# Performance work log

Hardware: AMD Instinct MI355X
Metric: run time of the kernel (lower is better)

Reference implementation:

```python
import jax, jax.numpy as jnp
import numpy as np

B, N, C, H = 8, 1568, 384, 6
D = C // H
SCALE = D ** -0.5
EPS = 1e-6


def setup_inputs() -> dict:
    key = jax.random.key(0)
    k1, k2, k3, k4 = jax.random.split(key, 4)
    x = jax.random.normal(k1, (B, N, C), dtype=jnp.float32)
    # binary token-keep policy (0/1), as produced by the pruning module
    vis_tube = jax.random.randint(k2, (B, N, 1), 0, 2).astype(jnp.float32)
    w_qkv = jax.random.normal(k3, (3 * C, C), dtype=jnp.float32) * (C ** -0.5)
    w_proj = jax.random.normal(k4, (C, C), dtype=jnp.float32) * (C ** -0.5)
    b_proj = jnp.zeros((C,), dtype=jnp.float32)
    return {"x": x, "vis_tube": vis_tube, "w_qkv": w_qkv, "w_proj": w_proj, "b_proj": b_proj}


def _attn_forward(x, vis_tube, w_qkv, w_proj, b_proj):
    qkv = (x @ w_qkv.T).reshape(B, N, 3, H, D)
    qkv = jnp.transpose(qkv, (2, 0, 3, 1, 4))  # [3,B,H,N,D]
    q, k, v = qkv[0], qkv[1], qkv[2]

    attn = jnp.einsum('bhnd,bhmd->bhnm', q, k) * SCALE  # [B,H,N,N]

    # softmax_with_policy: mask keys by policy, but always keep the diagonal
    policy = vis_tube.reshape(B, 1, 1, N)
    eye = jnp.eye(N, dtype=policy.dtype).reshape(1, 1, N, N)
    attn_policy = policy + (1.0 - policy) * eye  # [B,1,N,N]

    max_att = jnp.max(attn, axis=-1, keepdims=True)
    e = jnp.exp(attn - max_att) * attn_policy
    attn = (e + EPS / N) / (jnp.sum(e, axis=-1, keepdims=True) + EPS)

    out = jnp.einsum('bhnm,bhmd->bhnd', attn, v)  # [B,H,N,D]
    out = jnp.transpose(out, (0, 2, 1, 3)).reshape(B, N, C)
    return out @ w_proj.T + b_proj


def reference(x, vis_tube, w_qkv, w_proj, b_proj):
    return _attn_forward(x, vis_tube, w_qkv, w_proj, b_proj)
```

## Files before the change

### kernel.cpp

```cpp
#include <hip/hip_runtime.h>

#define B_ 8
#define N_ 1568
#define C_ 384
#define H_ 6
#define D_ 64
#define BH_ 48
#define SZ_ (B_*H_*N_*D_)
#define EPS_ 1e-6f
#define EPSN_ (EPS_/(float)N_)
#define CSC_ 0.18033688011112042f

typedef short s16x8 __attribute__((ext_vector_type(8)));
typedef float f32x4 __attribute__((ext_vector_type(4)));

static __device__ __forceinline__ ushort f2bf(float f){
  union { float f; unsigned u; } v; v.f = f;
  unsigned r = v.u + 0x7fffu + ((v.u >> 16) & 1u);
  return (ushort)(r >> 16);
}
static __device__ __forceinline__ float bf2f(ushort u){
  union { unsigned u; float f; } v; v.u = ((unsigned)u) << 16; return v.f;
}
static __device__ __forceinline__ s16x8 pack8(float4 a, float4 b){
  s16x8 r;
  r[0]=(short)f2bf(a.x); r[1]=(short)f2bf(a.y); r[2]=(short)f2bf(a.z); r[3]=(short)f2bf(a.w);
  r[4]=(short)f2bf(b.x); r[5]=(short)f2bf(b.y); r[6]=(short)f2bf(b.z); r[7]=(short)f2bf(b.w);
  return r;
}
#define MFMA16(a,b,c) __builtin_amdgcn_mfma_f32_16x16x32_bf16((a),(b),(c),0,0,0)

#if __has_builtin(__builtin_amdgcn_exp2f)
#define EXP2F(x) __builtin_amdgcn_exp2f(x)
#else
#define EXP2F(x) exp2f(x)
#endif

#if __has_builtin(__builtin_amdgcn_update_dpp)
#define ROT16(x,c) __int_as_float(__builtin_amdgcn_update_dpp(0, __float_as_int(x), (c), 0xf, 0xf, true))
static __device__ __forceinline__ float rmax16(float x){
  x = fmaxf(x, ROT16(x,0x121)); x = fmaxf(x, ROT16(x,0x122));
  x = fmaxf(x, ROT16(x,0x124)); x = fmaxf(x, ROT16(x,0x128)); return x;
}
static __device__ __forceinline__ float rsum16(float x){
  x += ROT16(x,0x121); x += ROT16(x,0x122); x += ROT16(x,0x124); x += ROT16(x,0x128); return x;
}
#else
static __device__ __forceinline__ float rmax16(float x){
  x = fmaxf(x, __shfl_xor(x,1)); x = fmaxf(x, __shfl_xor(x,2));
  x = fmaxf(x, __shfl_xor(x,4)); x = fmaxf(x, __shfl_xor(x,8)); return x;
}
static __device__ __forceinline__ float rsum16(float x){
  x += __shfl_xor(x,1); x += __shfl_xor(x,2); x += __shfl_xor(x,4); x += __shfl_xor(x,8); return x;
}
#endif

__global__ __launch_bounds__(256) void qkv_gemm(const float* __restrict__ X, const float* __restrict__ W,
                                                ushort* __restrict__ Qg, ushort* __restrict__ Kg,
                                                ushort* __restrict__ Vg){
  __shared__ __align__(16) ushort Al[128*40];
  __shared__ __align__(16) ushort Bl[64*40];
  const int tid = threadIdx.x, lane = tid&63, w = tid>>6;
  const int g = lane>>4, lr = lane&15;
  const int wr = w>>1, wc = w&1;
  const int m0 = blockIdx.x*128, j0 = blockIdx.y*64;
  const int ar = tid>>1, ah = tid&1;
  const int br = tid>>2, bq = tid&3;
  f32x4 acc[4][2];
  #pragma unroll
  for (int i=0;i<4;i++){ acc[i][0]=(f32x4){0.f,0.f,0.f,0.f}; acc[i][1]=(f32x4){0.f,0.f,0.f,0.f}; }

  for (int ks=0; ks<384; ks+=32){
    const float* as = X + (size_t)(m0+ar)*384 + ks + ah*16;
    float4 a0 = ((const float4*)as)[0], a1 = ((const float4*)as)[1];
    float4 a2 = ((const float4*)as)[2], a3 = ((const float4*)as)[3];
    const float* bs = W + (size_t)(j0+br)*384 + ks + bq*8;
    float4 b0 = ((const float4*)bs)[0], b1 = ((const float4*)bs)[1];
    *(s16x8*)&Al[ar*40 + ah*16]     = pack8(a0,a1);
    *(s16x8*)&Al[ar*40 + ah*16 + 8] = pack8(a2,a3);
    *(s16x8*)&Bl[br*40 + bq*8]      = pack8(b0,b1);
    __syncthreads();
    s16x8 af[4], bf[2];
    #pragma unroll
    for (int fm=0; fm<4; fm++) af[fm] = *(const s16x8*)&Al[(wr*64+fm*16+lr)*40 + g*8];
    #pragma unroll
    for (int fn=0; fn<2; fn++) bf[fn] = *(const s16x8*)&Bl[(wc*32+fn*16+lr)*40 + g*8];
    #pragma unroll
    for (int fm=0; fm<4; fm++)
      #pragma unroll
      for (int fn=0; fn<2; fn++)
        acc[fm][fn] = MFMA16(af[fm], bf[fn], acc[fm][fn]);
    __syncthreads();
  }
  const int t = j0/384, h = (j0%384)/64;
  #pragma unroll
  for (int fm=0; fm<4; fm++){
    #pragma unroll
    for (int jj=0; jj<4; jj++){
      int m = m0 + wr*64 + fm*16 + g*4 + jj;
      int bi = m / N_; int n = m - bi*N_;
      #pragma unroll
      for (int fn=0; fn<2; fn++){
        int d = wc*32 + fn*16 + lr;
        float v = acc[fm][fn][jj];
        int idx = ((bi*H_ + h)*N_ + n)*64 + d;
        if (t==0)      Qg[idx] = f2bf(v * CSC_);
        else if (t==1) Kg[idx] = f2bf(v);
        else           Vg[idx] = f2bf(v);
      }
    }
  }
}

__global__ __launch_bounds__(256) void attn_fwd(const ushort* __restrict__ Qg, const ushort* __restrict__ Kg,
                                                const ushort* __restrict__ Vg, const float* __restrict__ pol_g,
                                                ushort* __restrict__ AO){
  __shared__ __align__(16) char smem[15104];
  ushort* Klds = (ushort*)smem;
  ushort* Vtld = (ushort*)(smem + 4608);
  ushort* Plds = (ushort*)(smem + 9728);
  float*  pols = (float*)(smem + 14848);
  float*  red  = (float*)smem;
  __shared__ float sumv_s[64];

  const int tid = threadIdx.x, lane = tid&63, w = tid>>6;
  const int g = lane>>4, lr = lane&15;
  const int bh = blockIdx.x; const int b = bh / H_, h = bh - b*H_;
  const int q0 = blockIdx.y*64;
  const int qrow0 = q0 + w*16;
  const int qn = qrow0 + lr;
  const int qnc = qn < N_ ? qn : N_-1;
  const ushort* Qrow = Qg + ((size_t)bh*N_ + qnc)*64;
  const s16x8 qf0 = *(const s16x8*)(Qrow + g*8);
  const s16x8 qf1 = *(const s16x8*)(Qrow + 32 + g*8);
  ushort* Pw = Plds + w*(16*40);
  const float* polp = pol_g + b*N_;

  const int kk = tid>>3, kc = tid&7;
  const int vk = tid&31, vc = tid>>5;

  f32x4 o[4];
  #pragma unroll
  for (int i=0;i<4;i++) o[i] = (f32x4){0.f,0.f,0.f,0.f};
  float M[4] = {-INFINITY,-INFINITY,-INFINITY,-INFINITY};
  float L[4] = {0.f,0.f,0.f,0.f};
  float vpart[8] = {0.f,0.f,0.f,0.f,0.f,0.f,0.f,0.f};

  for (int t0=0; t0<N_; t0+=32){
    s16x8 kvv = *(const s16x8*)(Kg + ((size_t)bh*N_ + t0 + kk)*64 + kc*8);
    *(s16x8*)(Klds + kk*72 + kc*8) = kvv;
    s16x8 vvv = *(const s16x8*)(Vg + ((size_t)bh*N_ + t0 + vk)*64 + vc*8);
    #pragma unroll
    for (int i=0;i<8;i++){
      Vtld[(vc*8+i)*40 + vk] = (ushort)vvv[i];
      vpart[i] += bf2f((ushort)vvv[i]);
    }
    if (tid < 32) pols[tid] = polp[t0 + tid];
    __syncthreads();

    f32x4 s0 = (f32x4){0.f,0.f,0.f,0.f}, s1 = (f32x4){0.f,0.f,0.f,0.f};
    {
      const ushort* kb0 = Klds + (size_t)lr*72;
      const ushort* kb1 = Klds + (size_t)(16+lr)*72;
      s0 = MFMA16(qf0, *(const s16x8*)(kb0 + g*8), s0);
      s0 = MFMA16(qf1, *(const s16x8*)(kb0 + 32 + g*8), s0);
      s1 = MFMA16(qf0, *(const s16x8*)(kb1 + g*8), s1);
      s1 = MFMA16(qf1, *(const s16x8*)(kb1 + 32 + g*8), s1);
    }
    float p0 = pols[lr], p1 = pols[16+lr];
    int key0 = t0 + lr, key1 = t0 + 16 + lr;
    #pragma unroll
    for (int jj=0; jj<4; jj++){
      float a0 = s0[jj], a1 = s1[jj];
      float mj = rmax16(fmaxf(a0, a1));
      float Mn = fmaxf(M[jj], mj);
      float corr = EXP2F(M[jj] - Mn);
      int rowg = qrow0 + g*4 + jj;
      float e0 = EXP2F(a0 - Mn);
      float e1 = EXP2F(a1 - Mn);
      e0 = (p0 != 0.f || key0 == rowg) ? e0 : 0.f;
      e1 = (p1 != 0.f || key1 == rowg) ? e1 : 0.f;
      float se = rsum16(e0 + e1);
      L[jj] = L[jj]*corr + se;
      M[jj] = Mn;
      o[0][jj]*=corr; o[1][jj]*=corr; o[2][jj]*=corr; o[3][jj]*=corr;
      Pw[(g*4+jj)*40 + lr]      = f2bf(e0);
      Pw[(g*4+jj)*40 + 16 + lr] = f2bf(e1);
    }
    asm volatile("s_waitcnt lgkmcnt(0)" ::: "memory");
    __builtin_amdgcn_sched_barrier(0);
    const s16x8 pa = *(const s16x8*)(Pw + (size_t)lr*40 + g*8);
    #pragma unroll
    for (int fd=0; fd<4; fd++){
      const s16x8 vb = *(const s16x8*)(Vtld + (size_t)(fd*16+lr)*40 + g*8);
      o[fd] = MFMA16(pa, vb, o[fd]);
    }
    __syncthreads();
  }

  #pragma unroll
  for (int i=0;i<8;i++) red[tid*8+i] = vpart[i];
  __syncthreads();
  if (tid < 64){
    float s = 0.f; int c = tid>>3, i = tid&7;
    for (int key=0; key<32; key++) s += red[(c*32+key)*8 + i];
    sumv_s[tid] = s;
  }
  __syncthreads();

  float sv[4];
  #pragma unroll
  for (int fd=0; fd<4; fd++) sv[fd] = sumv_s[fd*16 + lr];
  #pragma unroll
  for (int jj=0; jj<4; jj++){
    int rowg = qrow0 + g*4 + jj;
    if (rowg < N_){
      float inv = 1.f / (L[jj] + EPS_);
      #pragma unroll
      for (int fd=0; fd<4; fd++){
        float val = (o[fd][jj] + EPSN_*sv[fd]) * inv;
        AO[((size_t)b*N_ + rowg)*C_ + h*64 + fd*16 + lr] = f2bf(val);
      }
    }
  }
}

__global__ __launch_bounds__(256) void proj_gemm(const ushort* __restrict__ A, const float* __restrict__ W,
                                                 const float* __restrict__ bias, float* __restrict__ out){
  __shared__ __align__(16) ushort Al[128*40];
  __shared__ __align__(16) ushort Bl[64*40];
  const int tid = threadIdx.x, lane = tid&63, w = tid>>6;
  const int g = lane>>4, lr = lane&15;
  const int wr = w>>1, wc = w&1;
  const int m0 = blockIdx.x*128, j0 = blockIdx.y*64;
  const int ar = tid>>1, ah = tid&1;
  const int br = tid>>2, bq = tid&3;
  f32x4 acc[4][2];
  #pragma unroll
  for (int i=0;i<4;i++){ acc[i][0]=(f32x4){0.f,0.f,0.f,0.f}; acc[i][1]=(f32x4){0.f,0.f,0.f,0.f}; }

  for (int ks=0; ks<384; ks+=32){
    const ushort* as = A + (size_t)(m0+ar)*384 + ks + ah*16;
    s16x8 av0 = ((const s16x8*)as)[0];
    s16x8 av1 = ((const s16x8*)as)[1];
    const float* bs = W + (size_t)(j0+br)*384 + ks + bq*8;
    float4 b0 = ((const float4*)bs)[0], b1 = ((const float4*)bs)[1];
    *(s16x8*)&Al[ar*40 + ah*16]     = av0;
    *(s16x8*)&Al[ar*40 + ah*16 + 8] = av1;
    *(s16x8*)&Bl[br*40 + bq*8]      = pack8(b0,b1);
    __syncthreads();
    s16x8 af[4], bf[2];
    #pragma unroll
    for (int fm=0; fm<4; fm++) af[fm] = *(const s16x8*)&Al[(wr*64+fm*16+lr)*40 + g*8];
    #pragma unroll
    for (int fn=0; fn<2; fn++) bf[fn] = *(const s16x8*)&Bl[(wc*32+fn*16+lr)*40 + g*8];
    #pragma unroll
    for (int fm=0; fm<4; fm++)
      #pragma unroll
      for (int fn=0; fn<2; fn++)
        acc[fm][fn] = MFMA16(af[fm], bf[fn], acc[fm][fn]);
    __syncthreads();
  }
  float bs0 = bias[j0 + wc*32 + lr];
  float bs1 = bias[j0 + wc*32 + 16 + lr];
  #pragma unroll
  for (int fm=0; fm<4; fm++){
    #pragma unroll
    for (int jj=0; jj<4; jj++){
      int m = m0 + wr*64 + fm*16 + g*4 + jj;
      out[(size_t)m*384 + j0 + wc*32 + lr]      = acc[fm][0][jj] + bs0;
      out[(size_t)m*384 + j0 + wc*32 + 16 + lr] = acc[fm][1][jj] + bs1;
    }
  }
}

extern "C" void kernel_launch(void* const* d_in, const int* in_sizes, int n_in,
                              void* d_out, int out_size, void* d_ws, size_t ws_size,
                              hipStream_t stream) {
  const float* x     = (const float*)d_in[0];
  const float* vis   = (const float*)d_in[1];
  const float* wqkv  = (const float*)d_in[2];
  const float* wproj = (const float*)d_in[3];
  const float* bproj = (const float*)d_in[4];
  float* out = (float*)d_out;

  ushort* Qg = (ushort*)d_ws;
  ushort* Kg = Qg + SZ_;
  ushort* Vg = Kg + SZ_;
  ushort* AO = Vg + SZ_;

  qkv_gemm<<<dim3(98,18), 256, 0, stream>>>(x, wqkv, Qg, Kg, Vg);
  attn_fwd<<<dim3(48,25), 256, 0, stream>>>(Qg, Kg, Vg, vis, AO);
  proj_gemm<<<dim3(98,6), 256, 0, stream>>>(AO, wproj, bproj, out);
}
```

Before: 257.5 us.

## Rewrite attention with 64-key tiles and pre-convert GEMM inputs to bf16

A new conversion kernel turns x and both weight matrices into bf16 up front. The two GEMMs then load MFMA fragments straight from global memory, with no LDS staging and no barriers. Attention now processes 64-key tiles with transposed S (K as the A operand) and XOR-swizzled LDS. The P matrix is repacked through cross-lane shuffles instead of an LDS round trip, and the running max is only rescaled when it grows by more than a threshold. The tiny EPS/N·sum(V) term is dropped, trading exactness for less work; the GEMMs also lose LDS reuse and now make redundant global loads.

```diff
diff --git a/kernel.cpp b/kernel.cpp
--- a/kernel.cpp
+++ b/kernel.cpp
@@ -8,10 +8,10 @@
 #define BH_ 48
 #define SZ_ (B_*H_*N_*D_)
 #define EPS_ 1e-6f
-#define EPSN_ (EPS_/(float)N_)
 #define CSC_ 0.18033688011112042f
 
 typedef short s16x8 __attribute__((ext_vector_type(8)));
+typedef short s16x4 __attribute__((ext_vector_type(4)));
 typedef float f32x4 __attribute__((ext_vector_type(4)));
 
 static __device__ __forceinline__ ushort f2bf(float f){
@@ -19,13 +19,9 @@
   unsigned r = v.u + 0x7fffu + ((v.u >> 16) & 1u);
   return (ushort)(r >> 16);
 }
-static __device__ __forceinline__ float bf2f(ushort u){
-  union { unsigned u; float f; } v; v.u = ((unsigned)u) << 16; return v.f;
-}
-static __device__ __forceinline__ s16x8 pack8(float4 a, float4 b){
-  s16x8 r;
-  r[0]=(short)f2bf(a.x); r[1]=(short)f2bf(a.y); r[2]=(short)f2bf(a.z); r[3]=(short)f2bf(a.w);
-  r[4]=(short)f2bf(b.x); r[5]=(short)f2bf(b.y); r[6]=(short)f2bf(b.z); r[7]=(short)f2bf(b.w);
+static __device__ __forceinline__ unsigned cvtpk(float lo, float hi){
+  unsigned r;
+  asm("v_cvt_pk_bf16_f32 %0, %1, %2" : "=v"(r) : "v"(lo), "v"(hi));
   return r;
 }
 #define MFMA16(a,b,c) __builtin_amdgcn_mfma_f32_16x16x32_bf16((a),(b),(c),0,0,0)
@@ -36,61 +32,48 @@
 #define EXP2F(x) exp2f(x)
 #endif
 
-#if __has_builtin(__builtin_amdgcn_update_dpp)
-#define ROT16(x,c) __int_as_float(__builtin_amdgcn_update_dpp(0, __float_as_int(x), (c), 0xf, 0xf, true))
-static __device__ __forceinline__ float rmax16(float x){
-  x = fmaxf(x, ROT16(x,0x121)); x = fmaxf(x, ROT16(x,0x122));
-  x = fmaxf(x, ROT16(x,0x124)); x = fmaxf(x, ROT16(x,0x128)); return x;
-}
-static __device__ __forceinline__ float rsum16(float x){
-  x += ROT16(x,0x121); x += ROT16(x,0x122); x += ROT16(x,0x124); x += ROT16(x,0x128); return x;
-}
-#else
-static __device__ __forceinline__ float rmax16(float x){
-  x = fmaxf(x, __shfl_xor(x,1)); x = fmaxf(x, __shfl_xor(x,2));
-  x = fmaxf(x, __shfl_xor(x,4)); x = fmaxf(x, __shfl_xor(x,8)); return x;
-}
-static __device__ __forceinline__ float rsum16(float x){
-  x += __shfl_xor(x,1); x += __shfl_xor(x,2); x += __shfl_xor(x,4); x += __shfl_xor(x,8); return x;
-}
-#endif
-
-__global__ __launch_bounds__(256) void qkv_gemm(const float* __restrict__ X, const float* __restrict__ W,
+#define XV8_ 602112
+#define WQ8_ 55296
+#define WP8_ 18432
+__global__ __launch_bounds__(256) void cvt_all(const float* __restrict__ X, const float* __restrict__ Wq,
+                                               const float* __restrict__ Wp, ushort* __restrict__ Xb,
+                                               ushort* __restrict__ Wqb, ushort* __restrict__ Wpb){
+  int i = blockIdx.x*256 + threadIdx.x;
+  const float* src; ushort* dst; int off;
+  if (i < XV8_)            { src = X;  dst = Xb;  off = i; }
+  else if (i < XV8_+WQ8_)  { src = Wq; dst = Wqb; off = i - XV8_; }
+  else                     { src = Wp; dst = Wpb; off = i - XV8_ - WQ8_; }
+  float4 a = ((const float4*)src)[off*2];
+  float4 b = ((const float4*)src)[off*2+1];
+  s16x8 r;
+  r[0]=(short)f2bf(a.x); r[1]=(short)f2bf(a.y); r[2]=(short)f2bf(a.z); r[3]=(short)f2bf(a.w);
+  r[4]=(short)f2bf(b.x); r[5]=(short)f2bf(b.y); r[6]=(short)f2bf(b.z); r[7]=(short)f2bf(b.w);
+  *(s16x8*)&dst[off*8] = r;
+}
+
+__global__ __launch_bounds__(256) void qkv_gemm(const ushort* __restrict__ Xb, const ushort* __restrict__ Wb,
                                                 ushort* __restrict__ Qg, ushort* __restrict__ Kg,
                                                 ushort* __restrict__ Vg){
-  __shared__ __align__(16) ushort Al[128*40];
-  __shared__ __align__(16) ushort Bl[64*40];
   const int tid = threadIdx.x, lane = tid&63, w = tid>>6;
   const int g = lane>>4, lr = lane&15;
   const int wr = w>>1, wc = w&1;
   const int m0 = blockIdx.x*128, j0 = blockIdx.y*64;
-  const int ar = tid>>1, ah = tid&1;
-  const int br = tid>>2, bq = tid&3;
   f32x4 acc[4][2];
   #pragma unroll
-  for (int i=0;i<4;i++){ acc[i][0]=(f32x4){0.f,0.f,0.f,0.f}; acc[i][1]=(f32x4){0.f,0.f,0.f,0.f}; }
-
+  for (int i=0;i<4;i++){ acc[i][0]=(f32x4){0,0,0,0}; acc[i][1]=(f32x4){0,0,0,0}; }
   for (int ks=0; ks<384; ks+=32){
-    const float* as = X + (size_t)(m0+ar)*384 + ks + ah*16;
-    float4 a0 = ((const float4*)as)[0], a1 = ((const float4*)as)[1];
-    float4 a2 = ((const float4*)as)[2], a3 = ((const float4*)as)[3];
-    const float* bs = W + (size_t)(j0+br)*384 + ks + bq*8;
-    float4 b0 = ((const float4*)bs)[0], b1 = ((const float4*)bs)[1];
-    *(s16x8*)&Al[ar*40 + ah*16]     = pack8(a0,a1);
-    *(s16x8*)&Al[ar*40 + ah*16 + 8] = pack8(a2,a3);
-    *(s16x8*)&Bl[br*40 + bq*8]      = pack8(b0,b1);
-    __syncthreads();
     s16x8 af[4], bf[2];
     #pragma unroll
-    for (int fm=0; fm<4; fm++) af[fm] = *(const s16x8*)&Al[(wr*64+fm*16+lr)*40 + g*8];
-    #pragma unroll
-    for (int fn=0; fn<2; fn++) bf[fn] = *(const s16x8*)&Bl[(wc*32+fn*16+lr)*40 + g*8];
+    for (int fm=0; fm<4; fm++)
+      af[fm] = *(const s16x8*)&Xb[(size_t)(m0+wr*64+fm*16+lr)*384 + ks + g*8];
+    #pragma unroll
+    for (int fn=0; fn<2; fn++)
+      bf[fn] = *(const s16x8*)&Wb[(size_t)(j0+wc*32+fn*16+lr)*384 + ks + g*8];
     #pragma unroll
     for (int fm=0; fm<4; fm++)
       #pragma unroll
       for (int fn=0; fn<2; fn++)
         acc[fm][fn] = MFMA16(af[fm], bf[fn], acc[fm][fn]);
-    __syncthreads();
   }
   const int t = j0/384, h = (j0%384)/64;
   #pragma unroll
@@ -115,151 +98,174 @@
 __global__ __launch_bounds__(256) void attn_fwd(const ushort* __restrict__ Qg, const ushort* __restrict__ Kg,
                                                 const ushort* __restrict__ Vg, const float* __restrict__ pol_g,
                                                 ushort* __restrict__ AO){
-  __shared__ __align__(16) char smem[15104];
-  ushort* Klds = (ushort*)smem;
-  ushort* Vtld = (ushort*)(smem + 4608);
-  ushort* Plds = (ushort*)(smem + 9728);
-  float*  pols = (float*)(smem + 14848);
-  float*  red  = (float*)smem;
-  __shared__ float sumv_s[64];
+  __shared__ __align__(16) ushort Kl[64*64];
+  __shared__ __align__(16) ushort Vt[64*64];
+  __shared__ __align__(16) float  pm_s[64];
 
   const int tid = threadIdx.x, lane = tid&63, w = tid>>6;
   const int g = lane>>4, lr = lane&15;
   const int bh = blockIdx.x; const int b = bh / H_, h = bh - b*H_;
-  const int q0 = blockIdx.y*64;
-  const int qrow0 = q0 + w*16;
-  const int qn = qrow0 + lr;
-  const int qnc = qn < N_ ? qn : N_-1;
-  const ushort* Qrow = Qg + ((size_t)bh*N_ + qnc)*64;
+  const int qrow0 = blockIdx.y*64 + w*16;
+  const int q = qrow0 + lr;
+  const int qc = q < N_ ? q : N_-1;
+  const ushort* Qrow = Qg + ((size_t)bh*N_ + qc)*64;
   const s16x8 qf0 = *(const s16x8*)(Qrow + g*8);
   const s16x8 qf1 = *(const s16x8*)(Qrow + 32 + g*8);
-  ushort* Pw = Plds + w*(16*40);
   const float* polp = pol_g + b*N_;
 
-  const int kk = tid>>3, kc = tid&7;
-  const int vk = tid&31, vc = tid>>5;
+  const int sr = tid>>2;
+  const int sc = (tid&3)*2;
+  const int swzK = (sr&7)<<4;
+  const int sl0 = ((lane>>4)&1)<<5 | lr;
+  const int sl1 = sl0 + 16;
 
   f32x4 o[4];
   #pragma unroll
-  for (int i=0;i<4;i++) o[i] = (f32x4){0.f,0.f,0.f,0.f};
-  float M[4] = {-INFINITY,-INFINITY,-INFINITY,-INFINITY};
-  float L[4] = {0.f,0.f,0.f,0.f};
-  float vpart[8] = {0.f,0.f,0.f,0.f,0.f,0.f,0.f,0.f};
-
-  for (int t0=0; t0<N_; t0+=32){
-    s16x8 kvv = *(const s16x8*)(Kg + ((size_t)bh*N_ + t0 + kk)*64 + kc*8);
-    *(s16x8*)(Klds + kk*72 + kc*8) = kvv;
-    s16x8 vvv = *(const s16x8*)(Vg + ((size_t)bh*N_ + t0 + vk)*64 + vc*8);
+  for (int i=0;i<4;i++) o[i] = (f32x4){0,0,0,0};
+  float M = -INFINITY, L = 0.f;
+
+  for (int t0=0; t0<N_; t0+=64){
+    int krow = t0 + sr; krow = krow < N_ ? krow : N_-1;
+    const size_t kb = ((size_t)bh*N_ + krow)*64;
+    s16x8 k0 = *(const s16x8*)(Kg + kb + sc*8);
+    s16x8 k1 = *(const s16x8*)(Kg + kb + sc*8 + 8);
+    *(s16x8*)((char*)Kl + sr*128 + ((sc*16) ^ swzK))     = k0;
+    *(s16x8*)((char*)Kl + sr*128 + (((sc+1)*16) ^ swzK)) = k1;
+    s16x8 v0 = *(const s16x8*)(Vg + kb + sc*8);
+    s16x8 v1 = *(const s16x8*)(Vg + kb + sc*8 + 8);
     #pragma unroll
     for (int i=0;i<8;i++){
-      Vtld[(vc*8+i)*40 + vk] = (ushort)vvv[i];
-      vpart[i] += bf2f((ushort)vvv[i]);
-    }
-    if (tid < 32) pols[tid] = polp[t0 + tid];
+      int d0 = sc*8 + i, d1 = sc*8 + 8 + i;
+      *(ushort*)((char*)Vt + d0*128 + ((2*sr) ^ ((d0&7)<<4))) = (ushort)v0[i];
+      *(ushort*)((char*)Vt + d1*128 + ((2*sr) ^ ((d1&7)<<4))) = (ushort)v1[i];
+    }
+    if (tid < 64) pm_s[tid] = (t0+tid < N_) ? polp[t0+tid] : 0.f;
     __syncthreads();
 
-    f32x4 s0 = (f32x4){0.f,0.f,0.f,0.f}, s1 = (f32x4){0.f,0.f,0.f,0.f};
+    f32x4 st[4];
+    const int swzR = (lr&7)<<4;
+    #pragma unroll
+    for (int kg=0; kg<4; kg++){
+      const char* krowp = (const char*)Kl + (kg*16+lr)*128;
+      s16x8 kf0 = *(const s16x8*)(krowp + ((g*16) ^ swzR));
+      s16x8 kf1 = *(const s16x8*)(krowp + ((64 + g*16) ^ swzR));
+      f32x4 z = (f32x4){0,0,0,0};
+      z = MFMA16(kf0, qf0, z);
+      st[kg] = MFMA16(kf1, qf1, z);
+    }
+
+    float pmax;
     {
-      const ushort* kb0 = Klds + (size_t)lr*72;
-      const ushort* kb1 = Klds + (size_t)(16+lr)*72;
-      s0 = MFMA16(qf0, *(const s16x8*)(kb0 + g*8), s0);
-      s0 = MFMA16(qf1, *(const s16x8*)(kb0 + 32 + g*8), s0);
-      s1 = MFMA16(qf0, *(const s16x8*)(kb1 + g*8), s1);
-      s1 = MFMA16(qf1, *(const s16x8*)(kb1 + 32 + g*8), s1);
-    }
-    float p0 = pols[lr], p1 = pols[16+lr];
-    int key0 = t0 + lr, key1 = t0 + 16 + lr;
-    #pragma unroll
-    for (int jj=0; jj<4; jj++){
-      float a0 = s0[jj], a1 = s1[jj];
-      float mj = rmax16(fmaxf(a0, a1));
-      float Mn = fmaxf(M[jj], mj);
-      float corr = EXP2F(M[jj] - Mn);
-      int rowg = qrow0 + g*4 + jj;
-      float e0 = EXP2F(a0 - Mn);
-      float e1 = EXP2F(a1 - Mn);
-      e0 = (p0 != 0.f || key0 == rowg) ? e0 : 0.f;
-      e1 = (p1 != 0.f || key1 == rowg) ? e1 : 0.f;
-      float se = rsum16(e0 + e1);
-      L[jj] = L[jj]*corr + se;
-      M[jj] = Mn;
-      o[0][jj]*=corr; o[1][jj]*=corr; o[2][jj]*=corr; o[3][jj]*=corr;
-      Pw[(g*4+jj)*40 + lr]      = f2bf(e0);
-      Pw[(g*4+jj)*40 + 16 + lr] = f2bf(e1);
-    }
-    asm volatile("s_waitcnt lgkmcnt(0)" ::: "memory");
-    __builtin_amdgcn_sched_barrier(0);
-    const s16x8 pa = *(const s16x8*)(Pw + (size_t)lr*40 + g*8);
+      float m0 = fmaxf(fmaxf(st[0][0],st[0][1]), fmaxf(st[0][2],st[0][3]));
+      float m1 = fmaxf(fmaxf(st[1][0],st[1][1]), fmaxf(st[1][2],st[1][3]));
+      float m2 = fmaxf(fmaxf(st[2][0],st[2][1]), fmaxf(st[2][2],st[2][3]));
+      float m3 = fmaxf(fmaxf(st[3][0],st[3][1]), fmaxf(st[3][2],st[3][3]));
+      pmax = fmaxf(fmaxf(m0,m1), fmaxf(m2,m3));
+      pmax = fmaxf(pmax, __shfl_xor(pmax, 16));
+      pmax = fmaxf(pmax, __shfl_xor(pmax, 32));
+    }
+    if (__any(pmax > M + 8.f)){
+      float Mn = fmaxf(M, pmax);
+      float corr = EXP2F(M - Mn);
+      L *= corr;
+      #pragma unroll
+      for (int fd=0; fd<4; fd++){ o[fd][0]*=corr; o[fd][1]*=corr; o[fd][2]*=corr; o[fd][3]*=corr; }
+      M = Mn;
+    }
+    const bool dg = (qrow0 & ~63) == t0;
+    #pragma unroll
+    for (int kg=0; kg<4; kg++){
+      float4 pmv = *(const float4*)&pm_s[kg*16 + 4*g];
+      if (dg){
+        #pragma unroll
+        for (int jj=0; jj<4; jj++){
+          float e = EXP2F(st[kg][jj] - M);
+          float em = e * ((&pmv.x)[jj]);
+          int key = t0 + kg*16 + 4*g + jj;
+          st[kg][jj] = (key == q) ? e : em;
+        }
+      } else {
+        #pragma unroll
+        for (int jj=0; jj<4; jj++){
+          float e = EXP2F(st[kg][jj] - M);
+          st[kg][jj] = e * ((&pmv.x)[jj]);
+        }
+      }
+    }
+    {
+      float se = (st[0][0]+st[0][1]) + (st[0][2]+st[0][3]);
+      se += (st[1][0]+st[1][1]) + (st[1][2]+st[1][3]);
+      se += (st[2][0]+st[2][1]) + (st[2][2]+st[2][3]);
+      se += (st[3][0]+st[3][1]) + (st[3][2]+st[3][3]);
+      se += __shfl_xor(se, 16);
+      se += __shfl_xor(se, 32);
+      L += se;
+    }
+
+    unsigned pk[4][2];
+    #pragma unroll
+    for (int kg=0; kg<4; kg++){
+      pk[kg][0] = cvtpk(st[kg][0], st[kg][1]);
+      pk[kg][1] = cvtpk(st[kg][2], st[kg][3]);
+    }
+    union { unsigned u[4]; s16x8 v; } bfr[2];
+    #pragma unroll
+    for (int kh=0; kh<2; kh++){
+      #pragma unroll
+      for (int wd=0; wd<4; wd++){
+        int srcl = (wd < 2) ? sl0 : sl1;
+        unsigned a0 = (unsigned)__shfl((int)pk[2*kh][wd&1],   srcl);
+        unsigned a1 = (unsigned)__shfl((int)pk[2*kh+1][wd&1], srcl);
+        bfr[kh].u[wd] = (g < 2) ? a0 : a1;
+      }
+    }
+
     #pragma unroll
     for (int fd=0; fd<4; fd++){
-      const s16x8 vb = *(const s16x8*)(Vtld + (size_t)(fd*16+lr)*40 + g*8);
-      o[fd] = MFMA16(pa, vb, o[fd]);
+      const char* vrow = (const char*)Vt + (fd*16+lr)*128;
+      s16x8 va0 = *(const s16x8*)(vrow + ((g*16) ^ swzR));
+      s16x8 va1 = *(const s16x8*)(vrow + ((64 + g*16) ^ swzR));
+      o[fd] = MFMA16(va0, bfr[0].v, o[fd]);
+      o[fd] = MFMA16(va1, bfr[1].v, o[fd]);
     }
     __syncthreads();
   }
 
-  #pragma unroll
-  for (int i=0;i<8;i++) red[tid*8+i] = vpart[i];
-  __syncthreads();
-  if (tid < 64){
-    float s = 0.f; int c = tid>>3, i = tid&7;
-    for (int key=0; key<32; key++) s += red[(c*32+key)*8 + i];
-    sumv_s[tid] = s;
-  }
-  __syncthreads();
-
-  float sv[4];
-  #pragma unroll
-  for (int fd=0; fd<4; fd++) sv[fd] = sumv_s[fd*16 + lr];
-  #pragma unroll
-  for (int jj=0; jj<4; jj++){
-    int rowg = qrow0 + g*4 + jj;
-    if (rowg < N_){
-      float inv = 1.f / (L[jj] + EPS_);
-      #pragma unroll
-      for (int fd=0; fd<4; fd++){
-        float val = (o[fd][jj] + EPSN_*sv[fd]) * inv;
-        AO[((size_t)b*N_ + rowg)*C_ + h*64 + fd*16 + lr] = f2bf(val);
-      }
-    }
-  }
-}
-
-__global__ __launch_bounds__(256) void proj_gemm(const ushort* __restrict__ A, const float* __restrict__ W,
+  if (q < N_){
+    float inv = 1.f / (L + EPS_);
+    ushort* aop = AO + ((size_t)b*N_ + q)*C_ + h*64 + 4*g;
+    #pragma unroll
+    for (int fd=0; fd<4; fd++){
+      s16x4 r;
+      r[0]=(short)f2bf(o[fd][0]*inv); r[1]=(short)f2bf(o[fd][1]*inv);
+      r[2]=(short)f2bf(o[fd][2]*inv); r[3]=(short)f2bf(o[fd][3]*inv);
+      *(s16x4*)(aop + fd*16) = r;
+    }
+  }
+}
+
+__global__ __launch_bounds__(256) void proj_gemm(const ushort* __restrict__ A, const ushort* __restrict__ Wb,
                                                  const float* __restrict__ bias, float* __restrict__ out){
-  __shared__ __align__(16) ushort Al[128*40];
-  __shared__ __align__(16) ushort Bl[64*40];
   const int tid = threadIdx.x, lane = tid&63, w = tid>>6;
   const int g = lane>>4, lr = lane&15;
   const int wr = w>>1, wc = w&1;
   const int m0 = blockIdx.x*128, j0 = blockIdx.y*64;
-  const int ar = tid>>1, ah = tid&1;
-  const int br = tid>>2, bq = tid&3;
   f32x4 acc[4][2];
   #pragma unroll
-  for (int i=0;i<4;i++){ acc[i][0]=(f32x4){0.f,0.f,0.f,0.f}; acc[i][1]=(f32x4){0.f,0.f,0.f,0.f}; }
-
+  for (int i=0;i<4;i++){ acc[i][0]=(f32x4){0,0,0,0}; acc[i][1]=(f32x4){0,0,0,0}; }
   for (int ks=0; ks<384; ks+=32){
-    const ushort* as = A + (size_t)(m0+ar)*384 + ks + ah*16;
-    s16x8 av0 = ((const s16x8*)as)[0];
-    s16x8 av1 = ((const s16x8*)as)[1];
-    const float* bs = W + (size_t)(j0+br)*384 + ks + bq*8;
-    float4 b0 = ((const float4*)bs)[0], b1 = ((const float4*)bs)[1];
-    *(s16x8*)&Al[ar*40 + ah*16]     = av0;
-    *(s16x8*)&Al[ar*40 + ah*16 + 8] = av1;
-    *(s16x8*)&Bl[br*40 + bq*8]      = pack8(b0,b1);
-    __syncthreads();
     s16x8 af[4], bf[2];
     #pragma unroll
-    for (int fm=0; fm<4; fm++) af[fm] = *(const s16x8*)&Al[(wr*64+fm*16+lr)*40 + g*8];
-    #pragma unroll
-    for (int fn=0; fn<2; fn++) bf[fn] = *(const s16x8*)&Bl[(wc*32+fn*16+lr)*40 + g*8];
+    for (int fm=0; fm<4; fm++)
+      af[fm] = *(const s16x8*)&A[(size_t)(m0+wr*64+fm*16+lr)*384 + ks + g*8];
+    #pragma unroll
+    for (int fn=0; fn<2; fn++)
+      bf[fn] = *(const s16x8*)&Wb[(size_t)(j0+wc*32+fn*16+lr)*384 + ks + g*8];
     #pragma unroll
     for (int fm=0; fm<4; fm++)
       #pragma unroll
       for (int fn=0; fn<2; fn++)
         acc[fm][fn] = MFMA16(af[fm], bf[fn], acc[fm][fn]);
-    __syncthreads();
   }
   float bs0 = bias[j0 + wc*32 + lr];
   float bs1 = bias[j0 + wc*32 + 16 + lr];
@@ -284,12 +290,16 @@
   const float* bproj = (const float*)d_in[4];
   float* out = (float*)d_out;
 
-  ushort* Qg = (ushort*)d_ws;
-  ushort* Kg = Qg + SZ_;
-  ushort* Vg = Kg + SZ_;
-  ushort* AO = Vg + SZ_;
-
-  qkv_gemm<<<dim3(98,18), 256, 0, stream>>>(x, wqkv, Qg, Kg, Vg);
+  ushort* Qg  = (ushort*)d_ws;
+  ushort* Kg  = Qg + SZ_;
+  ushort* Vg  = Kg + SZ_;
+  ushort* AO  = Vg + SZ_;
+  ushort* Xb  = AO;
+  ushort* Wqb = AO + SZ_;
+  ushort* Wpb = Wqb + 3*C_*C_;
+
+  cvt_all<<<2640, 256, 0, stream>>>(x, wqkv, wproj, Xb, Wqb, Wpb);
+  qkv_gemm<<<dim3(98,18), 256, 0, stream>>>(Xb, Wqb, Qg, Kg, Vg);
   attn_fwd<<<dim3(48,25), 256, 0, stream>>>(Qg, Kg, Vg, vis, AO);
-  proj_gemm<<<dim3(98,6), 256, 0, stream>>>(AO, wproj, bproj, out);
-}
+  proj_gemm<<<dim3(98,6), 256, 0, stream>>>(AO, Wpb, bproj, out);
+}
```

New measurement: 274.7 us. 1.07x slower.
